# Optimization experiments

Measured on AMD Instinct MI355X. Metric: run time of the kernel, lower is better.

The kernel has to match this reference:

```python
import jax, jax.numpy as jnp
import numpy as np

N_NODES = 50000
N_EDGES = 500000
N_GRAPHS = 16
C_IN = 2
CO_T = 64
CO_S = 16
K = 3


def conv_glu(x, w, b):
    # x: (N, Cin, T), w: (2*Cout, Cin, K), b: (2*Cout,) -> (N, Cout, T-K+1)
    y = jax.lax.conv_general_dilated(x, w, (1,), 'VALID',
                                     dimension_numbers=('NCH', 'OIH', 'NCH'))
    y = y + b[None, :, None]
    a, g = jnp.split(y, 2, axis=1)
    return a * jax.nn.sigmoid(g)


def gcn_relu(x, W, b, row, col, n_nodes):
    # GCNConv with self-loops, unit edge weights, applied to all T slices at once.
    # x: (N, Cin, T), W: (Cin, Cout), b: (Cout,)
    xw = jnp.einsum('nct,cd->ndt', x, W)  # (N, Cout, T)
    deg = jnp.zeros((n_nodes,), x.dtype).at[col].add(1.0) + 1.0  # +1 self loop
    dinv = deg ** -0.5
    coef = (dinv[row] * dinv[col])[:, None, None]
    msg = xw[row] * coef                   # (E, Cout, T) gather
    agg = jax.ops.segment_sum(msg, col, num_segments=n_nodes)
    agg = agg + xw * (dinv ** 2)[:, None, None]  # self-loop term
    return jax.nn.relu(agg + b[None, :, None])


def gap(x, batch, n_graphs):
    # global mean pool over nodes per graph; x: (N, C, T) -> (B, C, T)
    s = jax.ops.segment_sum(x, batch, num_segments=n_graphs)
    cnt = jax.ops.segment_sum(jnp.ones((x.shape[0],), x.dtype), batch, num_segments=n_graphs)
    return s / jnp.maximum(cnt, 1.0)[:, None, None]


def setup_inputs() -> dict:
    key = jax.random.key(0)
    ks = jax.random.split(key, 16)
    x = jax.random.normal(ks[0], (N_NODES, C_IN, 12), dtype=jnp.float32)
    edge_index = jax.random.randint(ks[1], (2, N_EDGES), 0, N_NODES)
    batch = jnp.sort(jax.random.randint(ks[2], (N_NODES,), 0, N_GRAPHS))

    def conv_p(k, cin, cout):
        k1, k2 = jax.random.split(k)
        fan = cin * K
        bound = 1.0 / np.sqrt(fan)
        w = jax.random.uniform(k1, (2 * cout, cin, K), jnp.float32, -bound, bound)
        b = jax.random.uniform(k2, (2 * cout,), jnp.float32, -bound, bound)
        return w, b

    w_t1a, b_t1a = conv_p(ks[3], C_IN, CO_T)
    w_t1b, b_t1b = conv_p(ks[4], CO_S, CO_T)
    w_t2a, b_t2a = conv_p(ks[5], CO_T, CO_T)
    w_t2b, b_t2b = conv_p(ks[6], CO_S, CO_T)

    def gcn_p(k, cin, cout):
        k1, k2 = jax.random.split(k)
        w = jax.random.normal(k1, (cin, cout), jnp.float32) * (1.0 / np.sqrt(cin))
        b = jnp.zeros((cout,), jnp.float32)
        return w, b

    w_s1, bb_s1 = gcn_p(ks[7], CO_T, CO_S)
    w_s2, bb_s2 = gcn_p(ks[8], CO_T, CO_S)

    return dict(x=x, edge_index=edge_index, batch=batch,
                w_t1a=w_t1a, b_t1a=b_t1a, w_s1=w_s1, bb_s1=bb_s1,
                w_t1b=w_t1b, b_t1b=b_t1b, w_t2a=w_t2a, b_t2a=b_t2a,
                w_s2=w_s2, bb_s2=bb_s2, w_t2b=w_t2b, b_t2b=b_t2b)


def reference(x, edge_index, batch, w_t1a, b_t1a, w_s1, bb_s1, w_t1b, b_t1b,
              w_t2a, b_t2a, w_s2, bb_s2, w_t2b, b_t2b):
    row, col = edge_index[0], edge_index[1]
    h = conv_glu(x, w_t1a, b_t1a)                     # (N, 64, 10)
    h = gcn_relu(h, w_s1, bb_s1, row, col, N_NODES)   # (N, 16, 10)
    h = conv_glu(h, w_t1b, b_t1b)                     # (N, 64, 8)
    h = conv_glu(h, w_t2a, b_t2a)                     # (N, 64, 6)
    h = gcn_relu(h, w_s2, bb_s2, row, col, N_NODES)   # (N, 16, 6)
    h = gap(h, batch, N_GRAPHS)                       # (B, 16, 6)
    out = conv_glu(h, w_t2b, b_t2b)                   # (B, 64, 4)
    return out
```

## Files before the change

### kernel.cpp

```cpp
#include <hip/hip_runtime.h>
#include <hip/hip_bf16.h>


#define NN 50000
#define NE 500000
#define NG 16
#define CAP 64

typedef __attribute__((ext_vector_type(8))) short bf16x8;
typedef __attribute__((ext_vector_type(8))) unsigned short u16x8;
typedef __attribute__((ext_vector_type(4))) float f32x4;

__device__ __forceinline__ float sigf(float g) {
    return 1.0f / (1.0f + __expf(-g));
}

__device__ __forceinline__ void split_bf16(float f, short& hi, short& lo) {
    unsigned b = __float_as_uint(f);
    unsigned r = b + 0x7FFFu + ((b >> 16) & 1u);
    unsigned short h = (unsigned short)(r >> 16);
    float lf = f - __uint_as_float(((unsigned)h) << 16);
    hi = (short)h;
    lo = (short)(__float_as_uint(lf) >> 16);
}

__device__ __forceinline__ unsigned short to_bf16(float f) {
    unsigned b = __float_as_uint(f);
    unsigned r = b + 0x7FFFu + ((b >> 16) & 1u);
    return (unsigned short)(r >> 16);
}

__device__ __forceinline__ float from_bf16(unsigned short u) {
    return __uint_as_float(((unsigned)u) << 16);
}

__global__ void k_fill(const int* __restrict__ row, const int* __restrict__ col,
                       int* __restrict__ cnt, unsigned short* __restrict__ bucket,
                       int E)
{
    int e = blockIdx.x * 256 + threadIdx.x;
    if (e >= E) return;
    int c = col[e];
    int pos = atomicAdd(&cnt[c], 1);
    if (pos < CAP) bucket[(size_t)c * CAP + pos] = (unsigned short)row[e];
}

__global__ void k_dinv(const int* __restrict__ cnt, float* __restrict__ dinv, int n) {
    int i = blockIdx.x * 256 + threadIdx.x;
    if (i < n) dinv[i] = rsqrtf((float)cnt[i] + 1.0f);
}

__global__ void k_prep2(const float* __restrict__ w1b, const float* __restrict__ w2a,
                        const float* __restrict__ ws2,
                        unsigned short* __restrict__ A2h, unsigned short* __restrict__ A2l,
                        unsigned short* __restrict__ A3h, unsigned short* __restrict__ A3l,
                        unsigned short* __restrict__ APh, unsigned short* __restrict__ APl)
{
    int idx = blockIdx.x * 256 + threadIdx.x;
    if (idx < 1024) {
        int lane = idx & 63; int r = idx >> 6; int s = r & 1; int T = r >> 1;
        int m = T * 16 + (lane & 15); int g = lane >> 4;
        for (int i = 0; i < 8; ++i) {
            int k = s * 32 + 8 * g + i;
            float w = 0.f;
            if (k < 48) { int ci = k & 15, kk = k >> 4; w = w1b[m * 48 + ci * 3 + kk]; }
            short h, l; split_bf16(w, h, l);
            A2h[idx * 8 + i] = (unsigned short)h; A2l[idx * 8 + i] = (unsigned short)l;
        }
    }
    if (idx < 3072) {
        int lane = idx & 63; int r = idx >> 6; int s = r % 6; int T = r / 6;
        int m = T * 16 + (lane & 15); int g = lane >> 4;
        for (int i = 0; i < 8; ++i) {
            int k = s * 32 + 8 * g + i;
            int ci = k & 63, kk = k >> 6;
            float w = w2a[m * 192 + ci * 3 + kk];
            short h, l; split_bf16(w, h, l);
            A3h[idx * 8 + i] = (unsigned short)h; A3l[idx * 8 + i] = (unsigned short)l;
        }
    }
    if (idx < 128) {
        int lane = idx & 63; int s = idx >> 6;
        int d = lane & 15; int g = lane >> 4;
        for (int i = 0; i < 8; ++i) {
            int co = s * 32 + 8 * g + i;
            float w = ws2[co * 16 + d];
            short h, l; split_bf16(w, h, l);
            APh[idx * 8 + i] = (unsigned short)h; APl[idx * 8 + i] = (unsigned short)l;
        }
    }
}

__global__ __launch_bounds__(256) void k_conv1_proj2(
    const float* __restrict__ x, const float* __restrict__ w,
    const float* __restrict__ b, const float* __restrict__ W1,
    const float* __restrict__ dinv, unsigned short* __restrict__ xwb, int nNodes)
{
    __shared__ float pk[64 * 28];
    __shared__ float bs[128];
    int tid = threadIdx.x;
    for (int i = tid; i < 1792; i += 256) {
        int c = i / 28, q = i - c * 28;
        float v;
        if (q < 6)       v = w[c * 6 + q];
        else if (q < 12) v = w[(c + 64) * 6 + (q - 6)];
        else             v = W1[c * 16 + (q - 12)];
        pk[i] = v;
    }
    if (tid < 128) bs[tid] = b[tid];
    __syncthreads();

    int idx = blockIdx.x * 256 + tid;
    if (idx >= nNodes * 5) return;
    int n = idx / 5, p = idx - n * 5;
    int t0 = 2 * p;

    float xq[2][4];
#pragma unroll
    for (int ci = 0; ci < 2; ++ci) {
        const float* xp = &x[n * 24 + ci * 12 + t0];
        float2 u0 = *(const float2*)(xp);
        float2 u1 = *(const float2*)(xp + 2);
        xq[ci][0] = u0.x; xq[ci][1] = u0.y; xq[ci][2] = u1.x; xq[ci][3] = u1.y;
    }

    float acc0[16], acc1[16];
#pragma unroll
    for (int d = 0; d < 16; ++d) { acc0[d] = 0.f; acc1[d] = 0.f; }

    for (int c = 0; c < 64; ++c) {
        const float* P = &pk[c * 28];
        float4 A = *(const float4*)(P);
        float4 B = *(const float4*)(P + 4);
        float4 C = *(const float4*)(P + 8);
        float bc = bs[c], bg = bs[c + 64];

        float a0 = bc, g0 = bg;
        a0 = fmaf(A.x, xq[0][0], a0); a0 = fmaf(A.y, xq[0][1], a0); a0 = fmaf(A.z, xq[0][2], a0);
        a0 = fmaf(A.w, xq[1][0], a0); a0 = fmaf(B.x, xq[1][1], a0); a0 = fmaf(B.y, xq[1][2], a0);
        g0 = fmaf(B.z, xq[0][0], g0); g0 = fmaf(B.w, xq[0][1], g0); g0 = fmaf(C.x, xq[0][2], g0);
        g0 = fmaf(C.y, xq[1][0], g0); g0 = fmaf(C.z, xq[1][1], g0); g0 = fmaf(C.w, xq[1][2], g0);
        float h0 = a0 * sigf(g0);

        float a1 = bc, g1 = bg;
        a1 = fmaf(A.x, xq[0][1], a1); a1 = fmaf(A.y, xq[0][2], a1); a1 = fmaf(A.z, xq[0][3], a1);
        a1 = fmaf(A.w, xq[1][1], a1); a1 = fmaf(B.x, xq[1][2], a1); a1 = fmaf(B.y, xq[1][3], a1);
        g1 = fmaf(B.z, xq[0][1], g1); g1 = fmaf(B.w, xq[0][2], g1); g1 = fmaf(C.x, xq[0][3], g1);
        g1 = fmaf(C.y, xq[1][1], g1); g1 = fmaf(C.z, xq[1][2], g1); g1 = fmaf(C.w, xq[1][3], g1);
        float h1 = a1 * sigf(g1);

        float4 D = *(const float4*)(P + 12);
        float4 E = *(const float4*)(P + 16);
        float4 F = *(const float4*)(P + 20);
        float4 G = *(const float4*)(P + 24);
        float wr[16] = {D.x, D.y, D.z, D.w, E.x, E.y, E.z, E.w,
                        F.x, F.y, F.z, F.w, G.x, G.y, G.z, G.w};
#pragma unroll
        for (int d = 0; d < 16; ++d) {
            acc0[d] = fmaf(wr[d], h0, acc0[d]);
            acc1[d] = fmaf(wr[d], h1, acc1[d]);
        }
    }
    float dv = dinv[n];
    u16x8 p0, p1, p2_, p3_;
#pragma unroll
    for (int d = 0; d < 8; ++d) {
        p0[d]  = to_bf16(acc0[d] * dv);
        p1[d]  = to_bf16(acc0[d + 8] * dv);
        p2_[d] = to_bf16(acc1[d] * dv);
        p3_[d] = to_bf16(acc1[d + 8] * dv);
    }
    unsigned short* o = &xwb[n * 160 + t0 * 16];
    *(u16x8*)(o)      = p0;
    *(u16x8*)(o + 8)  = p1;
    *(u16x8*)(o + 16) = p2_;
    *(u16x8*)(o + 24) = p3_;
}

template <int W8>
__global__ __launch_bounds__(256) void k_gather_bf(
    const unsigned short* __restrict__ xs, const unsigned short* __restrict__ bucket,
    const int* __restrict__ cnt, const float* __restrict__ dinv,
    const float* __restrict__ bias, float* __restrict__ h, int total)
{
    constexpr int W = W8 * 8;
    int idx = blockIdx.x * 256 + threadIdx.x;
    if (idx >= total) return;
    int c = idx / W8, ch = idx - c * W8;
    const int deg = min(cnt[c], CAP);
    const size_t choff = (size_t)ch * 8;

    float acc[8];
#pragma unroll
    for (int i = 0; i < 8; ++i) acc[i] = 0.f;

    for (int j = 0; j < deg; j += 4) {
        ushort4 id4 = *(const ushort4*)&bucket[(size_t)c * CAP + j];
        {
            u16x8 v = *(const u16x8*)&xs[(size_t)id4.x * W + choff];
#pragma unroll
            for (int i = 0; i < 8; ++i) acc[i] += from_bf16(v[i]);
        }
        if (j + 1 < deg) {
            u16x8 v = *(const u16x8*)&xs[(size_t)id4.y * W + choff];
#pragma unroll
            for (int i = 0; i < 8; ++i) acc[i] += from_bf16(v[i]);
        }
        if (j + 2 < deg) {
            u16x8 v = *(const u16x8*)&xs[(size_t)id4.z * W + choff];
#pragma unroll
            for (int i = 0; i < 8; ++i) acc[i] += from_bf16(v[i]);
        }
        if (j + 3 < deg) {
            u16x8 v = *(const u16x8*)&xs[(size_t)id4.w * W + choff];
#pragma unroll
            for (int i = 0; i < 8; ++i) acc[i] += from_bf16(v[i]);
        }
    }

    const float dv = dinv[c];
    u16x8 sv = *(const u16x8*)&xs[(size_t)c * W + choff];
    const float* bp = &bias[(ch & 1) * 8];
    float4 b0 = *(const float4*)(bp);
    float4 b1 = *(const float4*)(bp + 4);
    float bb[8] = {b0.x, b0.y, b0.z, b0.w, b1.x, b1.y, b1.z, b1.w};
    float o[8];
#pragma unroll
    for (int i = 0; i < 8; ++i)
        o[i] = fmaxf(dv * (acc[i] + from_bf16(sv[i])) + bb[i], 0.f);
    float* hp = &h[(size_t)c * W + choff];
    *(float4*)(hp)     = make_float4(o[0], o[1], o[2], o[3]);
    *(float4*)(hp + 4) = make_float4(o[4], o[5], o[6], o[7]);
}

__global__ __launch_bounds__(256) void k_conv23_v17(
    const float* __restrict__ h2g,
    const unsigned short* __restrict__ A2h, const unsigned short* __restrict__ A2l,
    const float* __restrict__ b1b,
    const unsigned short* __restrict__ A3h, const unsigned short* __restrict__ A3l,
    const float* __restrict__ b2a,
    const unsigned short* __restrict__ APh, const unsigned short* __restrict__ APl,
    const float* __restrict__ dinv, unsigned short* __restrict__ xw2b)
{
    __shared__ unsigned short H[11520];

    const int tid  = threadIdx.x;
    const int wid  = tid >> 6;
    const int lane = tid & 63;
    const int base = blockIdx.x * 16;

    unsigned short* H2 = H;
    unsigned short* H3 = H;

    const int nn   = lane & 15;
    const int nb   = nn >> 3;
    const int tt   = nn & 7;
    const int g    = lane >> 4;
    const int rowb = g * 4;

    for (int i = tid; i < 640; i += 256) {
        int ns = i / 40, r4 = i - ns * 40;
        int t = r4 >> 2, ci0 = (r4 & 3) << 2;
        float4 v = *(const float4*)&h2g[(size_t)(base + ns) * 160 + t * 16 + ci0];
        int o = ns * 288 + t * 24 + ci0;
        *(ushort4*)&H2[o] = make_ushort4(to_bf16(v.x), to_bf16(v.y),
                                         to_bf16(v.z), to_bf16(v.w));
    }
    for (int z = tid; z < 192; z += 256) {
        int ns = z / 12, rem = z % 12;
        int rrow = 10 + rem / 6, c4 = (rem % 6) * 4;
        *(ushort4*)&H2[ns * 288 + rrow * 24 + c4] = make_ushort4(0, 0, 0, 0);
    }
    __syncthreads();

    f32x4 a2[8][2];
    {
        float4 b0 = *(const float4*)&b1b[wid * 16 + rowb];
        float4 b1 = *(const float4*)&b1b[(wid + 4) * 16 + rowb];
#pragma unroll
        for (int b = 0; b < 8; ++b) {
            a2[b][0] = (f32x4){b0.x, b0.y, b0.z, b0.w};
            a2[b][1] = (f32x4){b1.x, b1.y, b1.z, b1.w};
        }
    }

#pragma unroll
    for (int s = 0; s < 2; ++s) {
        const int cib = 8 * (g & 1);
        const int kk  = 2 * s + (g >> 1);
        bf16x8 ah0 = *(const bf16x8*)&A2h[((wid * 2 + s) * 64 + lane) * 8];
        bf16x8 al0 = *(const bf16x8*)&A2l[((wid * 2 + s) * 64 + lane) * 8];
        bf16x8 ah1 = *(const bf16x8*)&A2h[(((wid + 4) * 2 + s) * 64 + lane) * 8];
        bf16x8 al1 = *(const bf16x8*)&A2l[(((wid + 4) * 2 + s) * 64 + lane) * 8];
#pragma unroll
        for (int b = 0; b < 8; ++b) {
            const int o = (2 * b + nb) * 288 + (tt + kk) * 24 + cib;
            bf16x8 bh = *(const bf16x8*)&H2[o];
            a2[b][0] = __builtin_amdgcn_mfma_f32_16x16x32_bf16(ah0, bh, a2[b][0], 0, 0, 0);
            a2[b][0] = __builtin_amdgcn_mfma_f32_16x16x32_bf16(al0, bh, a2[b][0], 0, 0, 0);
            a2[b][1] = __builtin_amdgcn_mfma_f32_16x16x32_bf16(ah1, bh, a2[b][1], 0, 0, 0);
            a2[b][1] = __builtin_amdgcn_mfma_f32_16x16x32_bf16(al1, bh, a2[b][1], 0, 0, 0);
        }
    }
    __syncthreads();

    {
#pragma unroll
        for (int b = 0; b < 8; ++b) {
            const int wb = (2 * b + nb) * 720 + tt * 72 + wid * 16 + rowb;
            float v0 = a2[b][0][0] * sigf(a2[b][1][0]);
            float v1 = a2[b][0][1] * sigf(a2[b][1][1]);
            float v2 = a2[b][0][2] * sigf(a2[b][1][2]);
            float v3 = a2[b][0][3] * sigf(a2[b][1][3]);
            *(ushort4*)&H3[wb] = make_ushort4(to_bf16(v0), to_bf16(v1),
                                              to_bf16(v2), to_bf16(v3));
        }
        for (int z = tid; z < 512; z += 256) {
            int ns = z / 32, rem = z % 32;
            int rrow = 8 + rem / 16, c4 = (rem % 16) * 4;
            *(ushort4*)&H3[ns * 720 + rrow * 72 + c4] = make_ushort4(0, 0, 0, 0);
        }
    }
    __syncthreads();

    f32x4 a3[8][2];
    {
        float4 b0 = *(const float4*)&b2a[wid * 16 + rowb];
        float4 b1 = *(const float4*)&b2a[(wid + 4) * 16 + rowb];
#pragma unroll
        for (int b = 0; b < 8; ++b) {
            a3[b][0] = (f32x4){b0.x, b0.y, b0.z, b0.w};
            a3[b][1] = (f32x4){b1.x, b1.y, b1.z, b1.w};
        }
    }

#pragma unroll
    for (int s = 0; s < 6; ++s) {
        const int kbase = s * 32 + 8 * g;
        const int cib = kbase & 63;
        const int kk  = kbase >> 6;
        bf16x8 ah0 = *(const bf16x8*)&A3h[((wid * 6 + s) * 64 + lane) * 8];
        bf16x8 al0 = *(const bf16x8*)&A3l[((wid * 6 + s) * 64 + lane) * 8];
        bf16x8 ah1 = *(const bf16x8*)&A3h[(((wid + 4) * 6 + s) * 64 + lane) * 8];
        bf16x8 al1 = *(const bf16x8*)&A3l[(((wid + 4) * 6 + s) * 64 + lane) * 8];
#pragma unroll
        for (int b = 0; b < 8; ++b) {
            const int o = (2 * b + nb) * 720 + (tt + kk) * 72 + cib;
            bf16x8 bh = *(const bf16x8*)&H3[o];
            a3[b][0] = __builtin_amdgcn_mfma_f32_16x16x32_bf16(ah0, bh, a3[b][0], 0, 0, 0);
            a3[b][0] = __builtin_amdgcn_mfma_f32_16x16x32_bf16(al0, bh, a3[b][0], 0, 0, 0);
            a3[b][1] = __builtin_amdgcn_mfma_f32_16x16x32_bf16(ah1, bh, a3[b][1], 0, 0, 0);
            a3[b][1] = __builtin_amdgcn_mfma_f32_16x16x32_bf16(al1, bh, a3[b][1], 0, 0, 0);
        }
    }
    __syncthreads();

    {
#pragma unroll
        for (int b = 0; b < 8; ++b) {
            const int wb = (2 * b + nb) * 720 + tt * 72 + wid * 16 + rowb;
            float v0 = a3[b][0][0] * sigf(a3[b][1][0]);
            float v1 = a3[b][0][1] * sigf(a3[b][1][1]);
            float v2 = a3[b][0][2] * sigf(a3[b][1][2]);
            float v3 = a3[b][0][3] * sigf(a3[b][1][3]);
            *(ushort4*)&H3[wb] = make_ushort4(to_bf16(v0), to_bf16(v1),
                                              to_bf16(v2), to_bf16(v3));
        }
    }
    __syncthreads();

    f32x4 ap0 = (f32x4){0.f, 0.f, 0.f, 0.f};
    f32x4 ap1 = (f32x4){0.f, 0.f, 0.f, 0.f};
#pragma unroll
    for (int s = 0; s < 2; ++s) {
        const int cob = s * 32 + 8 * g;
        bf16x8 ah = *(const bf16x8*)&APh[(s * 64 + lane) * 8];
        bf16x8 al = *(const bf16x8*)&APl[(s * 64 + lane) * 8];
        {
            const int b = 2 * wid;
            const int o = (2 * b + nb) * 720 + tt * 72 + cob;
            bf16x8 bh = *(const bf16x8*)&H3[o];
            ap0 = __builtin_amdgcn_mfma_f32_16x16x32_bf16(ah, bh, ap0, 0, 0, 0);
            ap0 = __builtin_amdgcn_mfma_f32_16x16x32_bf16(al, bh, ap0, 0, 0, 0);
        }
        {
            const int b = 2 * wid + 1;
            const int o = (2 * b + nb) * 720 + tt * 72 + cob;
            bf16x8 bh = *(const bf16x8*)&H3[o];
            ap1 = __builtin_amdgcn_mfma_f32_16x16x32_bf16(ah, bh, ap1, 0, 0, 0);
            ap1 = __builtin_amdgcn_mfma_f32_16x16x32_bf16(al, bh, ap1, 0, 0, 0);
        }
    }

    if (tt < 6) {
        {
            const int ng = base + 2 * (2 * wid) + nb;
            const float dv = dinv[ng];
            ushort4 o = make_ushort4(to_bf16(ap0[0] * dv), to_bf16(ap0[1] * dv),
                                     to_bf16(ap0[2] * dv), to_bf16(ap0[3] * dv));
            *(ushort4*)&xw2b[(size_t)ng * 96 + tt * 16 + rowb] = o;
        }
        {
            const int ng = base + 2 * (2 * wid + 1) + nb;
            const float dv = dinv[ng];
            ushort4 o = make_ushort4(to_bf16(ap1[0] * dv), to_bf16(ap1[1] * dv),
                                     to_bf16(ap1[2] * dv), to_bf16(ap1[3] * dv));
            *(ushort4*)&xw2b[(size_t)ng * 96 + tt * 16 + rowb] = o;
        }
    }
}

__global__ __launch_bounds__(128) void k_pool(
    const float* __restrict__ h5, const int* __restrict__ batch,
    float* __restrict__ pool, int nNodes)
{
    int j = threadIdx.x;
    if (j >= 96) return;
    int n0 = blockIdx.x * 64;
    int n1 = min(n0 + 64, nNodes);
    int cur = batch[n0];
    float acc = 0.f;
    for (int n = n0; n < n1; ++n) {
        int g = batch[n];
        if (g != cur) { atomicAdd(&pool[cur * 96 + j], acc); acc = 0.f; cur = g; }
        acc += h5[(size_t)n * 96 + j];
    }
    atomicAdd(&pool[cur * 96 + j], acc);
}

__global__ __launch_bounds__(256) void k_final(
    const float* __restrict__ pool, const int* __restrict__ batch,
    const float* __restrict__ w, const float* __restrict__ b,
    float* __restrict__ out, int nNodes)
{
    __shared__ float m[96];
    __shared__ float ws[6144];
    __shared__ float bs[128];
    int g = blockIdx.x, tid = threadIdx.x;

    int lo = 0, hi = nNodes;
    while (lo < hi) { int mid = (lo + hi) >> 1; if (batch[mid] < g) lo = mid + 1; else hi = mid; }
    int lo2 = lo, hi2 = nNodes;
    while (lo2 < hi2) { int mid = (lo2 + hi2) >> 1; if (batch[mid] < g + 1) lo2 = mid + 1; else hi2 = mid; }
    float cntg = fmaxf((float)(lo2 - lo), 1.0f);

    if (tid < 96) m[tid] = pool[g * 96 + tid] / cntg;
    for (int i = tid; i < 6144; i += 256) ws[i] = w[i];
    if (tid < 128) bs[tid] = b[tid];
    __syncthreads();

    int c = tid >> 2, t = tid & 3;
    float a = bs[c], gg = bs[c + 64];
#pragma unroll
    for (int ci = 0; ci < 16; ++ci)
#pragma unroll
        for (int k = 0; k < 3; ++k) {
            float xv = m[(t + k) * 16 + ci];
            a  = fmaf(ws[c * 48 + ci * 3 + k],        xv, a);
            gg = fmaf(ws[(c + 64) * 48 + ci * 3 + k], xv, gg);
        }
    out[g * 256 + c * 4 + t] = a * sigf(gg);
}

extern "C" void kernel_launch(void* const* d_in, const int* in_sizes, int n_in,
                              void* d_out, int out_size, void* d_ws, size_t ws_size,
                              hipStream_t stream)
{
    const float* x      = (const float*)d_in[0];
    const int*   ei     = (const int*)  d_in[1];
    const int*   batch  = (const int*)  d_in[2];
    const float* w_t1a  = (const float*)d_in[3];
    const float* b_t1a  = (const float*)d_in[4];
    const float* w_s1   = (const float*)d_in[5];
    const float* bb_s1  = (const float*)d_in[6];
    const float* w_t1b  = (const float*)d_in[7];
    const float* b_t1b  = (const float*)d_in[8];
    const float* w_t2a  = (const float*)d_in[9];
    const float* b_t2a  = (const float*)d_in[10];
    const float* w_s2   = (const float*)d_in[11];
    const float* bb_s2  = (const float*)d_in[12];
    const float* w_t2b  = (const float*)d_in[13];
    const float* b_t2b  = (const float*)d_in[14];
    float* out = (float*)d_out;

    const int* row = ei;
    const int* col = ei + NE;

    float* F    = (float*)d_ws;
    float* h    = F;
    unsigned short* xwb = (unsigned short*)(h + (size_t)NN * 160);
    unsigned short* A2h = xwb + (size_t)NN * 160;
    unsigned short* A2l = A2h + 8192;
    unsigned short* A3h = A2l + 8192;
    unsigned short* A3l = A3h + 24576;
    unsigned short* APh = A3l + 24576;
    unsigned short* APl = APh + 1024;
    float* dinv = (float*)(APl + 1024);
    float* pool = dinv + NN;
    int*   cnt  = (int*)(pool + NG * 96);
    unsigned short* bucket = (unsigned short*)(cnt + NN);

    hipMemsetAsync(pool, 0, (size_t)(NG * 96 + NN) * sizeof(float), stream);

    k_fill<<<(NE + 255) / 256, 256, 0, stream>>>(row, col, cnt, bucket, NE);
    k_dinv<<<(NN + 255) / 256, 256, 0, stream>>>(cnt, dinv, NN);
    k_prep2<<<12, 256, 0, stream>>>(w_t1b, w_t2a, w_s2,
                                    A2h, A2l, A3h, A3l, APh, APl);

    k_conv1_proj2<<<(NN * 5 + 255) / 256, 256, 0, stream>>>(
        x, w_t1a, b_t1a, w_s1, dinv, xwb, NN);

    k_gather_bf<20><<<(NN * 20 + 255) / 256, 256, 0, stream>>>(
        xwb, bucket, cnt, dinv, bb_s1, h, NN * 20);

    k_conv23_v17<<<NN / 16, 256, 0, stream>>>(
        h, A2h, A2l, b_t1b, A3h, A3l, b_t2a, APh, APl, dinv, xwb);

    k_gather_bf<12><<<(NN * 12 + 255) / 256, 256, 0, stream>>>(
        xwb, bucket, cnt, dinv, bb_s2, h, NN * 12);

    k_pool<<<(NN + 63) / 64, 128, 0, stream>>>(h, batch, pool, NN);
    k_final<<<NG, 256, 0, stream>>>(pool, batch, w_t2b, b_t2b, out, NN);
}
```

Before: 237.5 us.

## Drop split-bf16 weight correction, store activations in bf16, inline dinv

New measurement: 222.6 us. 6.3% less time.

```diff
diff --git a/kernel.cpp b/kernel.cpp
--- a/kernel.cpp
+++ b/kernel.cpp
@@ -13,15 +13,6 @@
 
 __device__ __forceinline__ float sigf(float g) {
     return 1.0f / (1.0f + __expf(-g));
-}
-
-__device__ __forceinline__ void split_bf16(float f, short& hi, short& lo) {
-    unsigned b = __float_as_uint(f);
-    unsigned r = b + 0x7FFFu + ((b >> 16) & 1u);
-    unsigned short h = (unsigned short)(r >> 16);
-    float lf = f - __uint_as_float(((unsigned)h) << 16);
-    hi = (short)h;
-    lo = (short)(__float_as_uint(lf) >> 16);
 }
 
 __device__ __forceinline__ unsigned short to_bf16(float f) {
@@ -45,16 +36,11 @@
     if (pos < CAP) bucket[(size_t)c * CAP + pos] = (unsigned short)row[e];
 }
 
-__global__ void k_dinv(const int* __restrict__ cnt, float* __restrict__ dinv, int n) {
-    int i = blockIdx.x * 256 + threadIdx.x;
-    if (i < n) dinv[i] = rsqrtf((float)cnt[i] + 1.0f);
-}
-
 __global__ void k_prep2(const float* __restrict__ w1b, const float* __restrict__ w2a,
                         const float* __restrict__ ws2,
-                        unsigned short* __restrict__ A2h, unsigned short* __restrict__ A2l,
-                        unsigned short* __restrict__ A3h, unsigned short* __restrict__ A3l,
-                        unsigned short* __restrict__ APh, unsigned short* __restrict__ APl)
+                        unsigned short* __restrict__ A2h,
+                        unsigned short* __restrict__ A3h,
+                        unsigned short* __restrict__ APh)
 {
     int idx = blockIdx.x * 256 + threadIdx.x;
     if (idx < 1024) {
@@ -64,8 +50,7 @@
             int k = s * 32 + 8 * g + i;
             float w = 0.f;
             if (k < 48) { int ci = k & 15, kk = k >> 4; w = w1b[m * 48 + ci * 3 + kk]; }
-            short h, l; split_bf16(w, h, l);
-            A2h[idx * 8 + i] = (unsigned short)h; A2l[idx * 8 + i] = (unsigned short)l;
+            A2h[idx * 8 + i] = to_bf16(w);
         }
     }
     if (idx < 3072) {
@@ -74,9 +59,7 @@
         for (int i = 0; i < 8; ++i) {
             int k = s * 32 + 8 * g + i;
             int ci = k & 63, kk = k >> 6;
-            float w = w2a[m * 192 + ci * 3 + kk];
-            short h, l; split_bf16(w, h, l);
-            A3h[idx * 8 + i] = (unsigned short)h; A3l[idx * 8 + i] = (unsigned short)l;
+            A3h[idx * 8 + i] = to_bf16(w2a[m * 192 + ci * 3 + kk]);
         }
     }
     if (idx < 128) {
@@ -84,9 +67,7 @@
         int d = lane & 15; int g = lane >> 4;
         for (int i = 0; i < 8; ++i) {
             int co = s * 32 + 8 * g + i;
-            float w = ws2[co * 16 + d];
-            short h, l; split_bf16(w, h, l);
-            APh[idx * 8 + i] = (unsigned short)h; APl[idx * 8 + i] = (unsigned short)l;
+            APh[idx * 8 + i] = to_bf16(ws2[co * 16 + d]);
         }
     }
 }
@@ -94,7 +75,7 @@
 __global__ __launch_bounds__(256) void k_conv1_proj2(
     const float* __restrict__ x, const float* __restrict__ w,
     const float* __restrict__ b, const float* __restrict__ W1,
-    const float* __restrict__ dinv, unsigned short* __restrict__ xwb, int nNodes)
+    const int* __restrict__ cnt, unsigned short* __restrict__ xwb, int nNodes)
 {
     __shared__ float pk[64 * 28];
     __shared__ float bs[128];
@@ -161,7 +142,7 @@
             acc1[d] = fmaf(wr[d], h1, acc1[d]);
         }
     }
-    float dv = dinv[n];
+    float dv = rsqrtf((float)cnt[n] + 1.0f);
     u16x8 p0, p1, p2_, p3_;
 #pragma unroll
     for (int d = 0; d < 8; ++d) {
@@ -180,8 +161,8 @@
 template <int W8>
 __global__ __launch_bounds__(256) void k_gather_bf(
     const unsigned short* __restrict__ xs, const unsigned short* __restrict__ bucket,
-    const int* __restrict__ cnt, const float* __restrict__ dinv,
-    const float* __restrict__ bias, float* __restrict__ h, int total)
+    const int* __restrict__ cnt, const float* __restrict__ bias,
+    unsigned short* __restrict__ hb, int total)
 {
     constexpr int W = W8 * 8;
     int idx = blockIdx.x * 256 + threadIdx.x;
@@ -218,29 +199,25 @@
         }
     }
 
-    const float dv = dinv[c];
+    const float dv = rsqrtf((float)cnt[c] + 1.0f);
     u16x8 sv = *(const u16x8*)&xs[(size_t)c * W + choff];
     const float* bp = &bias[(ch & 1) * 8];
     float4 b0 = *(const float4*)(bp);
     float4 b1 = *(const float4*)(bp + 4);
     float bb[8] = {b0.x, b0.y, b0.z, b0.w, b1.x, b1.y, b1.z, b1.w};
-    float o[8];
+    u16x8 o;
 #pragma unroll
     for (int i = 0; i < 8; ++i)
-        o[i] = fmaxf(dv * (acc[i] + from_bf16(sv[i])) + bb[i], 0.f);
-    float* hp = &h[(size_t)c * W + choff];
-    *(float4*)(hp)     = make_float4(o[0], o[1], o[2], o[3]);
-    *(float4*)(hp + 4) = make_float4(o[4], o[5], o[6], o[7]);
-}
-
-__global__ __launch_bounds__(256) void k_conv23_v17(
-    const float* __restrict__ h2g,
-    const unsigned short* __restrict__ A2h, const unsigned short* __restrict__ A2l,
-    const float* __restrict__ b1b,
-    const unsigned short* __restrict__ A3h, const unsigned short* __restrict__ A3l,
-    const float* __restrict__ b2a,
-    const unsigned short* __restrict__ APh, const unsigned short* __restrict__ APl,
-    const float* __restrict__ dinv, unsigned short* __restrict__ xw2b)
+        o[i] = to_bf16(fmaxf(dv * (acc[i] + from_bf16(sv[i])) + bb[i], 0.f));
+    *(u16x8*)&hb[(size_t)c * W + choff] = o;
+}
+
+__global__ __launch_bounds__(256) void k_conv23_v18(
+    const unsigned short* __restrict__ h2b,
+    const unsigned short* __restrict__ A2h, const float* __restrict__ b1b,
+    const unsigned short* __restrict__ A3h, const float* __restrict__ b2a,
+    const unsigned short* __restrict__ APh, const int* __restrict__ cnt,
+    unsigned short* __restrict__ xw2b)
 {
     __shared__ unsigned short H[11520];
 
@@ -258,18 +235,22 @@
     const int g    = lane >> 4;
     const int rowb = g * 4;
 
-    for (int i = tid; i < 640; i += 256) {
-        int ns = i / 40, r4 = i - ns * 40;
-        int t = r4 >> 2, ci0 = (r4 & 3) << 2;
-        float4 v = *(const float4*)&h2g[(size_t)(base + ns) * 160 + t * 16 + ci0];
-        int o = ns * 288 + t * 24 + ci0;
-        *(ushort4*)&H2[o] = make_ushort4(to_bf16(v.x), to_bf16(v.y),
-                                         to_bf16(v.z), to_bf16(v.w));
-    }
-    for (int z = tid; z < 192; z += 256) {
-        int ns = z / 12, rem = z % 12;
-        int rrow = 10 + rem / 6, c4 = (rem % 6) * 4;
-        *(ushort4*)&H2[ns * 288 + rrow * 24 + c4] = make_ushort4(0, 0, 0, 0);
+    for (int i = tid; i < 320; i += 256) {
+        int ns = i / 20, rem = i - ns * 20;
+        int t = rem >> 1, ci0 = (rem & 1) * 8;
+        u16x8 v = *(const u16x8*)&h2b[(size_t)(base + ns) * 160 + t * 16 + ci0];
+        *(u16x8*)&H2[ns * 288 + t * 24 + ci0] = v;
+    }
+    for (int z = tid; z < 96; z += 256) {
+        int ns = z / 6, rem = z % 6;
+        int rrow = 10 + (rem >> 2), c8 = (rem % 2) * 8;
+        (void)rrow; (void)c8;
+    }
+    if (tid < 64) {
+        int ns = tid >> 2, rem = tid & 3;
+        int rrow = 10 + (rem >> 1), ci0 = (rem & 1) * 8;
+        u16x8 z8 = (u16x8){0,0,0,0,0,0,0,0};
+        *(u16x8*)&H2[ns * 288 + rrow * 24 + ci0] = z8;
     }
     __syncthreads();
 
@@ -289,17 +270,13 @@
         const int cib = 8 * (g & 1);
         const int kk  = 2 * s + (g >> 1);
         bf16x8 ah0 = *(const bf16x8*)&A2h[((wid * 2 + s) * 64 + lane) * 8];
-        bf16x8 al0 = *(const bf16x8*)&A2l[((wid * 2 + s) * 64 + lane) * 8];
         bf16x8 ah1 = *(const bf16x8*)&A2h[(((wid + 4) * 2 + s) * 64 + lane) * 8];
-        bf16x8 al1 = *(const bf16x8*)&A2l[(((wid + 4) * 2 + s) * 64 + lane) * 8];
 #pragma unroll
         for (int b = 0; b < 8; ++b) {
             const int o = (2 * b + nb) * 288 + (tt + kk) * 24 + cib;
             bf16x8 bh = *(const bf16x8*)&H2[o];
             a2[b][0] = __builtin_amdgcn_mfma_f32_16x16x32_bf16(ah0, bh, a2[b][0], 0, 0, 0);
-            a2[b][0] = __builtin_amdgcn_mfma_f32_16x16x32_bf16(al0, bh, a2[b][0], 0, 0, 0);
             a2[b][1] = __builtin_amdgcn_mfma_f32_16x16x32_bf16(ah1, bh, a2[b][1], 0, 0, 0);
-            a2[b][1] = __builtin_amdgcn_mfma_f32_16x16x32_bf16(al1, bh, a2[b][1], 0, 0, 0);
         }
     }
     __syncthreads();
@@ -340,17 +317,13 @@
         const int cib = kbase & 63;
         const int kk  = kbase >> 6;
         bf16x8 ah0 = *(const bf16x8*)&A3h[((wid * 6 + s) * 64 + lane) * 8];
-        bf16x8 al0 = *(const bf16x8*)&A3l[((wid * 6 + s) * 64 + lane) * 8];
         bf16x8 ah1 = *(const bf16x8*)&A3h[(((wid + 4) * 6 + s) * 64 + lane) * 8];
-        bf16x8 al1 = *(const bf16x8*)&A3l[(((wid + 4) * 6 + s) * 64 + lane) * 8];
 #pragma unroll
         for (int b = 0; b < 8; ++b) {
             const int o = (2 * b + nb) * 720 + (tt + kk) * 72 + cib;
             bf16x8 bh = *(const bf16x8*)&H3[o];
             a3[b][0] = __builtin_amdgcn_mfma_f32_16x16x32_bf16(ah0, bh, a3[b][0], 0, 0, 0);
-            a3[b][0] = __builtin_amdgcn_mfma_f32_16x16x32_bf16(al0, bh, a3[b][0], 0, 0, 0);
             a3[b][1] = __builtin_amdgcn_mfma_f32_16x16x32_bf16(ah1, bh, a3[b][1], 0, 0, 0);
-            a3[b][1] = __builtin_amdgcn_mfma_f32_16x16x32_bf16(al1, bh, a3[b][1], 0, 0, 0);
         }
     }
     __syncthreads();
@@ -375,34 +348,31 @@
     for (int s = 0; s < 2; ++s) {
         const int cob = s * 32 + 8 * g;
         bf16x8 ah = *(const bf16x8*)&APh[(s * 64 + lane) * 8];
-        bf16x8 al = *(const bf16x8*)&APl[(s * 64 + lane) * 8];
         {
             const int b = 2 * wid;
             const int o = (2 * b + nb) * 720 + tt * 72 + cob;
             bf16x8 bh = *(const bf16x8*)&H3[o];
             ap0 = __builtin_amdgcn_mfma_f32_16x16x32_bf16(ah, bh, ap0, 0, 0, 0);
-            ap0 = __builtin_amdgcn_mfma_f32_16x16x32_bf16(al, bh, ap0, 0, 0, 0);
         }
         {
             const int b = 2 * wid + 1;
             const int o = (2 * b + nb) * 720 + tt * 72 + cob;
             bf16x8 bh = *(const bf16x8*)&H3[o];
             ap1 = __builtin_amdgcn_mfma_f32_16x16x32_bf16(ah, bh, ap1, 0, 0, 0);
-            ap1 = __builtin_amdgcn_mfma_f32_16x16x32_bf16(al, bh, ap1, 0, 0, 0);
         }
     }
 
     if (tt < 6) {
         {
             const int ng = base + 2 * (2 * wid) + nb;
-            const float dv = dinv[ng];
+            const float dv = rsqrtf((float)cnt[ng] + 1.0f);
             ushort4 o = make_ushort4(to_bf16(ap0[0] * dv), to_bf16(ap0[1] * dv),
                                      to_bf16(ap0[2] * dv), to_bf16(ap0[3] * dv));
             *(ushort4*)&xw2b[(size_t)ng * 96 + tt * 16 + rowb] = o;
         }
         {
             const int ng = base + 2 * (2 * wid + 1) + nb;
-            const float dv = dinv[ng];
+            const float dv = rsqrtf((float)cnt[ng] + 1.0f);
             ushort4 o = make_ushort4(to_bf16(ap1[0] * dv), to_bf16(ap1[1] * dv),
                                      to_bf16(ap1[2] * dv), to_bf16(ap1[3] * dv));
             *(ushort4*)&xw2b[(size_t)ng * 96 + tt * 16 + rowb] = o;
@@ -411,7 +381,7 @@
 }
 
 __global__ __launch_bounds__(128) void k_pool(
-    const float* __restrict__ h5, const int* __restrict__ batch,
+    const unsigned short* __restrict__ h5b, const int* __restrict__ batch,
     float* __restrict__ pool, int nNodes)
 {
     int j = threadIdx.x;
@@ -423,7 +393,7 @@
     for (int n = n0; n < n1; ++n) {
         int g = batch[n];
         if (g != cur) { atomicAdd(&pool[cur * 96 + j], acc); acc = 0.f; cur = g; }
-        acc += h5[(size_t)n * 96 + j];
+        acc += from_bf16(h5b[(size_t)n * 96 + j]);
     }
     atomicAdd(&pool[cur * 96 + j], acc);
 }
@@ -486,39 +456,33 @@
     const int* row = ei;
     const int* col = ei + NE;
 
-    float* F    = (float*)d_ws;
-    float* h    = F;
-    unsigned short* xwb = (unsigned short*)(h + (size_t)NN * 160);
-    unsigned short* A2h = xwb + (size_t)NN * 160;
-    unsigned short* A2l = A2h + 8192;
-    unsigned short* A3h = A2l + 8192;
-    unsigned short* A3l = A3h + 24576;
-    unsigned short* APh = A3l + 24576;
-    unsigned short* APl = APh + 1024;
-    float* dinv = (float*)(APl + 1024);
-    float* pool = dinv + NN;
+    unsigned short* U   = (unsigned short*)d_ws;
+    unsigned short* xwb = U;
+    unsigned short* hb  = xwb + (size_t)NN * 160;
+    unsigned short* A2h = hb + (size_t)NN * 160;
+    unsigned short* A3h = A2h + 8192;
+    unsigned short* APh = A3h + 24576;
+    float* pool = (float*)(APh + 1024);
     int*   cnt  = (int*)(pool + NG * 96);
     unsigned short* bucket = (unsigned short*)(cnt + NN);
 
     hipMemsetAsync(pool, 0, (size_t)(NG * 96 + NN) * sizeof(float), stream);
 
     k_fill<<<(NE + 255) / 256, 256, 0, stream>>>(row, col, cnt, bucket, NE);
-    k_dinv<<<(NN + 255) / 256, 256, 0, stream>>>(cnt, dinv, NN);
-    k_prep2<<<12, 256, 0, stream>>>(w_t1b, w_t2a, w_s2,
-                                    A2h, A2l, A3h, A3l, APh, APl);
+    k_prep2<<<12, 256, 0, stream>>>(w_t1b, w_t2a, w_s2, A2h, A3h, APh);
 
     k_conv1_proj2<<<(NN * 5 + 255) / 256, 256, 0, stream>>>(
-        x, w_t1a, b_t1a, w_s1, dinv, xwb, NN);
+        x, w_t1a, b_t1a, w_s1, cnt, xwb, NN);
 
     k_gather_bf<20><<<(NN * 20 + 255) / 256, 256, 0, stream>>>(
-        xwb, bucket, cnt, dinv, bb_s1, h, NN * 20);
-
-    k_conv23_v17<<<NN / 16, 256, 0, stream>>>(
-        h, A2h, A2l, b_t1b, A3h, A3l, b_t2a, APh, APl, dinv, xwb);
+        xwb, bucket, cnt, bb_s1, hb, NN * 20);
+
+    k_conv23_v18<<<NN / 16, 256, 0, stream>>>(
+        hb, A2h, b_t1b, A3h, b_t2a, APh, cnt, xwb);
 
     k_gather_bf<12><<<(NN * 12 + 255) / 256, 256, 0, stream>>>(
-        xwb, bucket, cnt, dinv, bb_s2, h, NN * 12);
-
-    k_pool<<<(NN + 63) / 64, 128, 0, stream>>>(h, batch, pool, NN);
+        xwb, bucket, cnt, bb_s2, hb, NN * 12);
+
+    k_pool<<<(NN + 63) / 64, 128, 0, stream>>>(hb, batch, pool, NN);
     k_final<<<NG, 256, 0, stream>>>(pool, batch, w_t2b, b_t2b, out, NN);
 }
```
